# Optimization experiments

Measured on AMD Instinct MI355X. Metric: run time of the kernel, lower is better.

The kernel has to match this reference:

```python
import jax, jax.numpy as jnp
import numpy as np

DIM, HEADS, K_MAX, K_MIN = 512, 8, 32, 4
DH = DIM // HEADS


def _conv1x1(x, w, b=None):
    # 1x1 Conv2d == pointwise linear over channels: [B,C,H,W] x [O,C] -> [B,O,H,W]
    y = jnp.einsum('bchw,oc->bohw', x, w)
    if b is not None:
        y = y + b[None, :, None, None]
    return y


def setup_inputs() -> dict:
    key = jax.random.key(0)
    ks = jax.random.split(key, 8)
    B, C, H, W = 2, DIM, 64, 64
    s = lambda fan: 1.0 / np.sqrt(fan)
    x = jax.random.normal(ks[0], (B, C, H, W), jnp.float32)
    w_qkv = jax.random.normal(ks[1], (3 * C, C), jnp.float32) * s(C)   # qkv conv, bias=False
    w_proj = jax.random.normal(ks[2], (C, C), jnp.float32) * s(C)      # proj conv
    b_proj = jax.random.normal(ks[3], (C,), jnp.float32) * s(C)
    w_g1 = jax.random.normal(ks[4], (C // 4, C), jnp.float32) * s(C)   # gate conv 1
    b_g1 = jax.random.normal(ks[5], (C // 4,), jnp.float32) * s(C)
    w_g2 = jax.random.normal(ks[6], (1, C // 4), jnp.float32) * s(C // 4)  # gate conv 2
    b_g2 = jnp.full((1,), -1.0, jnp.float32)  # nn.init.constant_(gate[-2].bias, -1.0)
    return {"x": x, "w_qkv": w_qkv, "w_proj": w_proj, "b_proj": b_proj,
            "w_g1": w_g1, "b_g1": b_g1, "w_g2": w_g2, "b_g2": b_g2}


def reference(x, w_qkv, w_proj, b_proj, w_g1, b_g1, w_g2, b_g2):
    B, C, H, W = x.shape
    N = H * W
    qkv = _conv1x1(x, w_qkv)                              # [B,3C,H,W]
    q, k, v = jnp.split(qkv, 3, axis=1)

    def rs(t):  # [B,C,H,W] -> [B,heads,N,dh]
        return t.reshape(B, HEADS, DH, N).transpose(0, 1, 3, 2)

    q, k, v = rs(q), rs(k), rs(v)
    sim = jnp.einsum('bhid,bhjd->bhij', q, k) / np.sqrt(DH)  # [B,h,N,N]

    # adaptive tau gate -> per-query dynamic k
    tau = jax.nn.sigmoid(_conv1x1(jax.nn.relu(_conv1x1(x, w_g1, b_g1)), w_g2, b_g2))
    tau = tau.reshape(B, 1, N)
    k_dyn = jnp.clip((tau * K_MAX).astype(jnp.int32), K_MIN, K_MAX)  # [B,1,N]

    topk_val, topk_idx = jax.lax.top_k(sim, K_MAX)         # [B,h,N,K], sorted descending
    mask = jnp.arange(K_MAX)[None, None, None, :] < k_dyn[..., None]  # [B,1,N,K] (bcast over h)
    topk_val = jnp.where(mask, topk_val, -jnp.inf)
    attn = jax.nn.softmax(topk_val, axis=-1)               # [B,h,N,K]

    # gather values: gathered[b,h,i,kk,:] = v[b,h,topk_idx[b,h,i,kk],:]
    bi = jnp.arange(B)[:, None, None, None]
    hi = jnp.arange(HEADS)[None, :, None, None]
    gathered = v[bi, hi, topk_idx]                         # [B,h,N,K,dh]
    out = jnp.einsum('bhnk,bhnkd->bhnd', attn, gathered)   # [B,h,N,dh]

    out = out.transpose(0, 1, 3, 2).reshape(B, C, H, W)
    out = _conv1x1(out, w_proj, b_proj)                    # proj (proj_drop=0)
    return x + out
```

## Files before the change

### kernel.cpp

```cpp
#include <hip/hip_runtime.h>
#include <math.h>

#define XSTRIDE  2097152u
#define G1STRIDE 524288u

typedef _Float16 f16;
typedef f16   f16x8  __attribute__((ext_vector_type(8)));
typedef float f32x16 __attribute__((ext_vector_type(16)));
typedef unsigned int u32;
typedef unsigned short u16;

#define WS_QH 0u
#define WS_QL 2097152u
#define WS_KH 4194304u
#define WS_KL 6291456u
#define WS_VB 8388608u
#define WS_G1 10485760u
#define WS_KD 11534336u
#define WS_CI 11542528u

template<int EPI>
__global__ __launch_bounds__(256)
void gemm_kernel(const float* __restrict__ A, const float* __restrict__ B,
                 const float* __restrict__ bias, const float* __restrict__ resid,
                 void* P0, void* P1, void* P2, void* P3, void* P4)
{
    const int tid = threadIdx.x;
    const int tm = tid & 15;
    const int tn = tid >> 4;
    const int m0 = blockIdx.y * 128;
    const int n0 = blockIdx.x * 128;
    const int b  = blockIdx.z;

    const float* Bb = B + (size_t)b * XSTRIDE;

    __shared__ float As[16][132];
    __shared__ float Bs[16][132];

    float acc[8][8];
    #pragma unroll
    for (int i = 0; i < 8; ++i)
        #pragma unroll
        for (int j = 0; j < 8; ++j) acc[i][j] = 0.0f;

    for (int k0 = 0; k0 < 512; k0 += 16) {
        {
            int id = tid * 2;
            #pragma unroll
            for (int r = 0; r < 2; ++r, ++id) {
                int m = id >> 2, kq = (id & 3) * 4;
                float4 v = *(const float4*)(A + (size_t)(m0 + m) * 512 + k0 + kq);
                As[kq + 0][m] = v.x; As[kq + 1][m] = v.y;
                As[kq + 2][m] = v.z; As[kq + 3][m] = v.w;
            }
        }
        if (EPI != 2) {
            int id = tid * 2;
            #pragma unroll
            for (int r = 0; r < 2; ++r, ++id) {
                int kk = id >> 5, nq = (id & 31) * 4;
                *(float4*)(&Bs[kk][nq]) =
                    *(const float4*)(Bb + (size_t)(k0 + kk) * 4096 + n0 + nq);
            }
        } else {
            const float* O0p = (const float*)P1;
            const float* O1p = (const float*)P2;
            const int hh = k0 >> 6, d0 = k0 & 63;
            int id = tid * 2;
            #pragma unroll
            for (int r = 0; r < 2; ++r, ++id) {
                int n = id >> 2, kq = (id & 3) * 4;
                int dd = d0 + kq;
                size_t rowp = ((size_t)((b * 8 + hh) * 4096) + n0 + n) * 32;
                const float* src = (dd < 32) ? (O0p + rowp + dd) : (O1p + rowp + dd - 32);
                float4 v = *(const float4*)src;
                Bs[kq + 0][n] = v.x; Bs[kq + 1][n] = v.y;
                Bs[kq + 2][n] = v.z; Bs[kq + 3][n] = v.w;
            }
        }
        __syncthreads();
        #pragma unroll
        for (int k = 0; k < 16; ++k) {
            float4 a0 = *(const float4*)(&As[k][tm * 8]);
            float4 a1 = *(const float4*)(&As[k][tm * 8 + 4]);
            float4 b0 = *(const float4*)(&Bs[k][tn * 8]);
            float4 b1 = *(const float4*)(&Bs[k][tn * 8 + 4]);
            float a[8] = {a0.x, a0.y, a0.z, a0.w, a1.x, a1.y, a1.z, a1.w};
            float bb[8] = {b0.x, b0.y, b0.z, b0.w, b1.x, b1.y, b1.z, b1.w};
            #pragma unroll
            for (int i = 0; i < 8; ++i)
                #pragma unroll
                for (int j = 0; j < 8; ++j)
                    acc[i][j] += a[i] * bb[j];
        }
        __syncthreads();
    }

    if (EPI == 0) {
        const int which = m0 >> 9;
        const int mm = (m0 & 511) + tm * 8;
        const int hh = mm >> 6, d0 = mm & 63;
        const size_t rowbase = (size_t)((b * 8 + hh) * 4096);
        if (which == 2) {
            f16* VB = (f16*)P4;
            #pragma unroll
            for (int j = 0; j < 8; ++j) {
                int n = n0 + tn * 8 + j;
                f16x8 v;
                #pragma unroll
                for (int i = 0; i < 8; ++i) v[i] = (f16)acc[i][j];
                *(f16x8*)(VB + (rowbase + n) * 64 + d0) = v;
            }
        } else {
            f16* DH = (f16*)(which ? P2 : P0);
            f16* DL = (f16*)(which ? P3 : P1);
            const float scale = which ? 1.0f : 0.125f;
            #pragma unroll
            for (int j = 0; j < 8; ++j) {
                int n = n0 + tn * 8 + j;
                f16x8 vh, vl;
                #pragma unroll
                for (int i = 0; i < 8; ++i) {
                    float xx = acc[i][j] * scale;
                    f16 hs = (f16)xx;
                    vh[i] = hs;
                    vl[i] = (f16)((xx - (float)hs) * 4096.0f);
                }
                *(f16x8*)(DH + (rowbase + n) * 64 + d0) = vh;
                *(f16x8*)(DL + (rowbase + n) * 64 + d0) = vl;
            }
        }
    } else if (EPI == 1) {
        float* G1 = (float*)P0;
        #pragma unroll
        for (int i = 0; i < 8; ++i) {
            int o = tm * 8 + i;
            float bi = bias[o];
            float* dst = G1 + (size_t)b * G1STRIDE + (size_t)o * 4096 + n0 + tn * 8;
            float v[8];
            #pragma unroll
            for (int j = 0; j < 8; ++j) v[j] = fmaxf(acc[i][j] + bi, 0.0f);
            *(float4*)(dst) = make_float4(v[0], v[1], v[2], v[3]);
            *(float4*)(dst + 4) = make_float4(v[4], v[5], v[6], v[7]);
        }
    } else {
        float* out = (float*)P0;
        #pragma unroll
        for (int i = 0; i < 8; ++i) {
            int o = m0 + tm * 8 + i;
            float bi = bias[o];
            size_t off = (size_t)b * XSTRIDE + (size_t)o * 4096 + n0 + tn * 8;
            float4 r0 = *(const float4*)(resid + off);
            float4 r1 = *(const float4*)(resid + off + 4);
            *(float4*)(out + off) = make_float4(acc[i][0] + bi + r0.x, acc[i][1] + bi + r0.y,
                                                acc[i][2] + bi + r0.z, acc[i][3] + bi + r0.w);
            *(float4*)(out + off + 4) = make_float4(acc[i][4] + bi + r1.x, acc[i][5] + bi + r1.y,
                                                    acc[i][6] + bi + r1.z, acc[i][7] + bi + r1.w);
        }
    }
}

__global__ __launch_bounds__(256)
void convert_kernel(const float* __restrict__ x,
                    f16* __restrict__ XTH, f16* __restrict__ XTL)
{
    __shared__ float T[64][65];
    const int b = blockIdx.z;
    const int n0 = blockIdx.x * 64, k0 = blockIdx.y * 64;
    const int tid = threadIdx.x;
    const float* xb = x + (size_t)b * XSTRIDE;

    {
        const int c = tid & 63, r = tid >> 6;
        #pragma unroll
        for (int i = 0; i < 16; ++i)
            T[r + i * 4][c] = xb[(size_t)(k0 + r + i * 4) * 4096 + n0 + c];
    }
    __syncthreads();
    const int n = tid >> 2, a = tid & 3;
    f16x8 vh[2], vl[2];
    #pragma unroll
    for (int p = 0; p < 2; ++p)
        #pragma unroll
        for (int j = 0; j < 8; ++j) {
            float v = T[a * 16 + p * 8 + j][n];
            f16 h = (f16)v;
            vh[p][j] = h;
            vl[p][j] = (f16)((v - (float)h) * 4096.0f);
        }
    size_t dst = ((size_t)(b * 4096) + n0 + n) * 512 + k0 + a * 16;
    *(f16x8*)(XTH + dst)     = vh[0];
    *(f16x8*)(XTH + dst + 8) = vh[1];
    *(f16x8*)(XTL + dst)     = vl[0];
    *(f16x8*)(XTL + dst + 8) = vl[1];
}

__global__ __launch_bounds__(256, 2)
void qkv_gemm(const float* __restrict__ W, const f16* __restrict__ XTH,
              const f16* __restrict__ XTL,
              f16* __restrict__ QH, f16* __restrict__ QL,
              f16* __restrict__ KH, f16* __restrict__ KL,
              f16* __restrict__ VB)
{
    __shared__ __align__(16) char smem[33792];
    f16* Ah = (f16*)smem;
    f16* Al = (f16*)(smem + 6144);
    f16* Bh = (f16*)(smem + 12288);
    f16* Bl = (f16*)(smem + 18432);

    const int tid  = threadIdx.x;
    const int wid  = tid >> 6, lane = tid & 63;
    const int ln   = lane & 31, g = lane >> 5;
    const int wm   = wid >> 1, wn = wid & 1;
    const int m0   = blockIdx.y * 128;
    const int n0   = blockIdx.x * 128;
    const int b    = blockIdx.z;

    const int sm = tid >> 1, sko = (tid & 1) * 8;
    const float* wsrc  = W + (size_t)(m0 + sm) * 512 + sko;
    const f16*  bsrcH = XTH + ((size_t)(b * 4096) + n0 + sm) * 512 + sko;
    const f16*  bsrcL = XTL + ((size_t)(b * 4096) + n0 + sm) * 512 + sko;

    f32x16 accH[2][2], accL[2][2];
    #pragma unroll
    for (int rb = 0; rb < 2; ++rb)
        #pragma unroll
        for (int cb = 0; cb < 2; ++cb)
            #pragma unroll
            for (int r = 0; r < 16; ++r) { accH[rb][cb][r] = 0.0f; accL[rb][cb][r] = 0.0f; }

    for (int k0 = 0; k0 < 512; k0 += 16) {
        {
            float4 v0 = *(const float4*)(wsrc + k0);
            float4 v1 = *(const float4*)(wsrc + k0 + 4);
            float vv[8] = {v0.x, v0.y, v0.z, v0.w, v1.x, v1.y, v1.z, v1.w};
            f16x8 hh, ll;
            #pragma unroll
            for (int j = 0; j < 8; ++j) {
                f16 h = (f16)vv[j];
                hh[j] = h;
                ll[j] = (f16)((vv[j] - (float)h) * 4096.0f);
            }
            *(f16x8*)(Ah + sm * 24 + sko) = hh;
            *(f16x8*)(Al + sm * 24 + sko) = ll;
            *(f16x8*)(Bh + sm * 24 + sko) = *(const f16x8*)(bsrcH + k0);
            *(f16x8*)(Bl + sm * 24 + sko) = *(const f16x8*)(bsrcL + k0);
        }
        __syncthreads();
        f16x8 a_h[2], a_l[2], b_h[2], b_l[2];
        #pragma unroll
        for (int rb = 0; rb < 2; ++rb) {
            int row = wm * 64 + rb * 32 + ln;
            a_h[rb] = *(const f16x8*)(Ah + row * 24 + g * 8);
            a_l[rb] = *(const f16x8*)(Al + row * 24 + g * 8);
        }
        #pragma unroll
        for (int cb = 0; cb < 2; ++cb) {
            int col = wn * 64 + cb * 32 + ln;
            b_h[cb] = *(const f16x8*)(Bh + col * 24 + g * 8);
            b_l[cb] = *(const f16x8*)(Bl + col * 24 + g * 8);
        }
        #pragma unroll
        for (int rb = 0; rb < 2; ++rb)
            #pragma unroll
            for (int cb = 0; cb < 2; ++cb) {
                accH[rb][cb] = __builtin_amdgcn_mfma_f32_32x32x16_f16(a_h[rb], b_h[cb], accH[rb][cb], 0, 0, 0);
                accL[rb][cb] = __builtin_amdgcn_mfma_f32_32x32x16_f16(a_h[rb], b_l[cb], accL[rb][cb], 0, 0, 0);
                accL[rb][cb] = __builtin_amdgcn_mfma_f32_32x32x16_f16(a_l[rb], b_h[cb], accL[rb][cb], 0, 0, 0);
            }
        __syncthreads();
    }

    const int which = m0 >> 9;
    const float scale = (which == 0) ? 0.125f : 1.0f;
    const int hh_ = ((m0 & 511) >> 6) + wm;
    const size_t rowb0 = (size_t)(b * 8 + hh_) * 4096 + n0 + wn * 64 + lane;
    float* E = (float*)smem + wid * 2112;

    #pragma unroll
    for (int rb = 0; rb < 2; ++rb) {
        #pragma unroll
        for (int cb = 0; cb < 2; ++cb)
            #pragma unroll
            for (int r = 0; r < 16; ++r) {
                int row = (r & 3) + 8 * (r >> 2) + 4 * g;
                E[row * 66 + cb * 32 + ln] =
                    accH[rb][cb][r] + accL[rb][cb][r] * (1.0f / 4096.0f);
            }
        __syncthreads();
        const int dbase = rb * 32;
        if (which == 2) {
            #pragma unroll
            for (int oct = 0; oct < 4; ++oct) {
                f16x8 vv;
                #pragma unroll
                for (int j = 0; j < 8; ++j) vv[j] = (f16)E[(oct * 8 + j) * 66 + lane];
                *(f16x8*)(VB + rowb0 * 64 + dbase + oct * 8) = vv;
            }
        } else {
            f16* DH = which ? KH : QH;
            f16* DL = which ? KL : QL;
            #pragma unroll
            for (int oct = 0; oct < 4; ++oct) {
                f16x8 vh, vl;
                #pragma unroll
                for (int j = 0; j < 8; ++j) {
                    float xx = E[(oct * 8 + j) * 66 + lane] * scale;
                    f16 h = (f16)xx;
                    vh[j] = h;
                    vl[j] = (f16)((xx - (float)h) * 4096.0f);
                }
                *(f16x8*)(DH + rowb0 * 64 + dbase + oct * 8) = vh;
                *(f16x8*)(DL + rowb0 * 64 + dbase + oct * 8) = vl;
            }
        }
        __syncthreads();
    }
}

__global__ __launch_bounds__(64)
void gate2_kernel(const float* __restrict__ G1, const float* __restrict__ w2,
                  const float* __restrict__ b2, int* __restrict__ KD)
{
    const int b = blockIdx.y;
    const int n = blockIdx.x * 64 + threadIdx.x;
    const float* g = G1 + (size_t)b * G1STRIDE + n;
    float z = b2[0];
    #pragma unroll 8
    for (int c = 0; c < 128; ++c) z += w2[c] * g[(size_t)c * 4096];
    float tau = 1.0f / (1.0f + expf(-z));
    int kd = (int)(tau * 32.0f);
    kd = min(32, max(4, kd));
    KD[b * 4096 + n] = kd;
}

#define LOAD_BF(B0,B1,B2,B3,B4,B5,B6,B7, KHP, KLP, CB) do {                   \
    const f16* _ph = (KHP) + (size_t)((CB) * 32 + ln) * 64 + g * 8;           \
    const f16* _pl = (KLP) + (size_t)((CB) * 32 + ln) * 64 + g * 8;           \
    B0 = *(const f16x8*)(_ph);      B1 = *(const f16x8*)(_ph + 16);           \
    B2 = *(const f16x8*)(_ph + 32); B3 = *(const f16x8*)(_ph + 48);           \
    B4 = *(const f16x8*)(_pl);      B5 = *(const f16x8*)(_pl + 16);           \
    B6 = *(const f16x8*)(_pl + 32); B7 = *(const f16x8*)(_pl + 48);           \
} while (0)

#define P1_SCAN() do {                                                        \
    u32 _m = 0;                                                               \
    _Pragma("unroll")                                                         \
    for (int _q = 0; _q < 16; ++_q) {                                         \
        float2 _v = *(const float2*)(srow + 2 * _q);                          \
        _m |= (_v.x > thr) ? (1u << (2 * _q)) : 0u;                           \
        _m |= (_v.y > thr) ? (1u << (2 * _q + 1)) : 0u;                       \
    }                                                                         \
    while (__ballot(_m != 0u)) {                                              \
        bool _act = (_m != 0u);                                               \
        int _j = __builtin_ctz(_m ? _m : 1u);                                 \
        float _c = _act ? srow[_j] : 0.0f;                                    \
        _m &= (_m - 1u);                                                      \
        if (_act && _c > thr) {                                               \
            _Pragma("unroll")                                                 \
            for (int _r = 31; _r >= 1; --_r)                                  \
                L[_r] = __builtin_amdgcn_fmed3f(_c, L[_r - 1], L[_r]);        \
            L[0] = fmaxf(L[0], _c);                                           \
        }                                                                     \
    }                                                                         \
    {                                                                         \
        float _th = L[31];                                                    \
        _Pragma("unroll")                                                     \
        for (int _r = 30; _r >= 0; --_r) _th = (kdm1 == _r) ? L[_r] : _th;    \
        thr = _th;                                                            \
    }                                                                         \
} while (0)

#define P2_SCAN(JBASE) do {                                                   \
    u32 _m = 0;                                                               \
    _Pragma("unroll")                                                         \
    for (int _q = 0; _q < 16; ++_q) {                                         \
        float2 _v = *(const float2*)(srow + 2 * _q);                          \
        _m |= (_v.x >= theta) ? (1u << (2 * _q)) : 0u;                        \
        _m |= (_v.y >= theta) ? (1u << (2 * _q + 1)) : 0u;                    \
    }                                                                         \
    while (__ballot(_m != 0u)) {                                              \
        bool _act = (_m != 0u);                                               \
        int _j = __builtin_ctz(_m ? _m : 1u);                                 \
        float _c = _act ? srow[_j] : 0.0f;                                    \
        _m &= (_m - 1u);                                                      \
        if (_act) {                                                           \
            bool _isGT = _c > theta;                                          \
            bool _doA = (_isGT || eqc < eqNeed) && cnt < 32;                  \
            if (_doA) {                                                       \
                cvp[cnt] = _c;                                                \
                cip[cnt] = (u16)((JBASE) + _j);                               \
                cnt++;                                                        \
                if (!_isGT) eqc++;                                            \
            }                                                                 \
        }                                                                     \
    }                                                                         \
} while (0)

__device__ __forceinline__ void score_from(
    f16x8 bh0, f16x8 bh1, f16x8 bh2, f16x8 bh3,
    f16x8 bl0, f16x8 bl1, f16x8 bl2, f16x8 bl3,
    const f16x8 ah[2][4], const f16x8 al[2][4],
    float* __restrict__ Ss, int ln, int g)
{
    __builtin_amdgcn_s_setprio(1);
    #pragma unroll
    for (int rb = 0; rb < 2; ++rb) {
        f32x16 acc, accL;
        #pragma unroll
        for (int r = 0; r < 16; ++r) { acc[r] = 0.0f; accL[r] = 0.0f; }
        acc  = __builtin_amdgcn_mfma_f32_32x32x16_f16(ah[rb][0], bh0, acc,  0, 0, 0);
        accL = __builtin_amdgcn_mfma_f32_32x32x16_f16(al[rb][0], bh0, accL, 0, 0, 0);
        accL = __builtin_amdgcn_mfma_f32_32x32x16_f16(ah[rb][0], bl0, accL, 0, 0, 0);
        acc  = __builtin_amdgcn_mfma_f32_32x32x16_f16(ah[rb][1], bh1, acc,  0, 0, 0);
        accL = __builtin_amdgcn_mfma_f32_32x32x16_f16(al[rb][1], bh1, accL, 0, 0, 0);
        accL = __builtin_amdgcn_mfma_f32_32x32x16_f16(ah[rb][1], bl1, accL, 0, 0, 0);
        acc  = __builtin_amdgcn_mfma_f32_32x32x16_f16(ah[rb][2], bh2, acc,  0, 0, 0);
        accL = __builtin_amdgcn_mfma_f32_32x32x16_f16(al[rb][2], bh2, accL, 0, 0, 0);
        accL = __builtin_amdgcn_mfma_f32_32x32x16_f16(ah[rb][2], bl2, accL, 0, 0, 0);
        acc  = __builtin_amdgcn_mfma_f32_32x32x16_f16(ah[rb][3], bh3, acc,  0, 0, 0);
        accL = __builtin_amdgcn_mfma_f32_32x32x16_f16(al[rb][3], bh3, accL, 0, 0, 0);
        accL = __builtin_amdgcn_mfma_f32_32x32x16_f16(ah[rb][3], bl3, accL, 0, 0, 0);
        #pragma unroll
        for (int r = 0; r < 16; ++r) {
            int riw = rb * 32 + (r & 3) + 8 * (r >> 2) + 4 * g;
            Ss[riw * 34 + ln] = acc[r] + accL[r] * (1.0f / 4096.0f);
        }
    }
    __builtin_amdgcn_s_setprio(0);
}

__global__ __launch_bounds__(64)
__attribute__((amdgpu_waves_per_eu(2, 2)))
void select_kernel(const f16* __restrict__ QH, const f16* __restrict__ QL,
                   const f16* __restrict__ KH, const f16* __restrict__ KL,
                   const int* __restrict__ KD,
                   float* __restrict__ CV, u16* __restrict__ CI)
{
    const int qt = blockIdx.x >> 1;
    const int hf = blockIdx.x & 1;
    const int h = blockIdx.y, b = blockIdx.z;
    const size_t base = (size_t)((b * 8 + h) * 4096) * 64;
    const int lane = threadIdx.x;
    const int ln = lane & 31, g = lane >> 5;
    const int nw = qt * 64;
    const int k0base = hf * 2048;

    const int kd = KD[b * 4096 + nw + lane];
    const int kdm1 = kd - 1;

    __shared__ float Ss[64 * 34];

    f16x8 ah[2][4], al[2][4];
    #pragma unroll
    for (int rb = 0; rb < 2; ++rb) {
        const f16* ph = QH + base + (size_t)(nw + rb * 32 + ln) * 64 + g * 8;
        const f16* pl = QL + base + (size_t)(nw + rb * 32 + ln) * 64 + g * 8;
        #pragma unroll
        for (int s = 0; s < 4; ++s) {
            ah[rb][s] = *(const f16x8*)(ph + s * 16);
            al[rb][s] = *(const f16x8*)(pl + s * 16);
        }
    }

    const float INF = __builtin_inff();
    const float* srow = &Ss[lane * 34];

    f16x8 c0, c1, c2, c3, c4, c5, c6, c7;
    f16x8 n0, n1, n2, n3, n4, n5, n6, n7;

    float L[32];
    #pragma unroll
    for (int r = 0; r < 32; ++r) L[r] = -INF;
    float thr = -INF;

    {
        const f16* kh0 = KH + base + (size_t)k0base * 64;
        const f16* kl0 = KL + base + (size_t)k0base * 64;
        LOAD_BF(c0, c1, c2, c3, c4, c5, c6, c7, kh0, kl0, 0);
        for (int t = 0; t < 32; ++t) {
            const f16* kh_t = KH + base + (size_t)(k0base + t * 64) * 64;
            const f16* kl_t = KL + base + (size_t)(k0base + t * 64) * 64;
            const int t1 = (t < 31) ? t + 1 : 31;
            const f16* kh_n = KH + base + (size_t)(k0base + t1 * 64) * 64;
            const f16* kl_n = KL + base + (size_t)(k0base + t1 * 64) * 64;
            LOAD_BF(n0, n1, n2, n3, n4, n5, n6, n7, kh_t, kl_t, 1);
            score_from(c0, c1, c2, c3, c4, c5, c6, c7, ah, al, Ss, ln, g);
            P1_SCAN();
            LOAD_BF(c0, c1, c2, c3, c4, c5, c6, c7, kh_n, kl_n, 0);
            score_from(n0, n1, n2, n3, n4, n5, n6, n7, ah, al, Ss, ln, g);
            P1_SCAN();
        }
    }
    const float theta = thr;
    int cntGT = 0;
    #pragma unroll
    for (int r = 0; r < 32; ++r) cntGT += ((r < kd) && (L[r] > theta)) ? 1 : 0;
    const int eqNeed = kd - cntGT;

    const size_t crow = (size_t)((b * 8 + h) * 4096 + nw + lane);
    float* cvp = CV + crow * 64 + hf * 32;
    u16*   cip = CI + crow * 64 + hf * 32;
    int cnt = 0, eqc = 0;

    {
        const f16* kh0 = KH + base + (size_t)k0base * 64;
        const f16* kl0 = KL + base + (size_t)k0base * 64;
        LOAD_BF(c0, c1, c2, c3, c4, c5, c6, c7, kh0, kl0, 0);
        for (int t = 0; t < 32; ++t) {
            const f16* kh_t = KH + base + (size_t)(k0base + t * 64) * 64;
            const f16* kl_t = KL + base + (size_t)(k0base + t * 64) * 64;
            const int t1 = (t < 31) ? t + 1 : 31;
            const f16* kh_n = KH + base + (size_t)(k0base + t1 * 64) * 64;
            const f16* kl_n = KL + base + (size_t)(k0base + t1 * 64) * 64;
            LOAD_BF(n0, n1, n2, n3, n4, n5, n6, n7, kh_t, kl_t, 1);
            score_from(c0, c1, c2, c3, c4, c5, c6, c7, ah, al, Ss, ln, g);
            P2_SCAN(k0base + t * 64);
            LOAD_BF(c0, c1, c2, c3, c4, c5, c6, c7, kh_n, kl_n, 0);
            score_from(n0, n1, n2, n3, n4, n5, n6, n7, ah, al, Ss, ln, g);
            P2_SCAN(k0base + t * 64 + 32);
        }
    }
}

__global__ __launch_bounds__(64)
void merge_kernel(const float* __restrict__ CV, const u16* __restrict__ CI,
                  const int* __restrict__ KD, const f16* __restrict__ VB,
                  float* __restrict__ O0, float* __restrict__ O1)
{
    const int tid = threadIdx.x;
    const size_t R0 = (size_t)blockIdx.x * 64;

    __shared__ float Lv[64][66];
    __shared__ u16   Li[64][66];
    __shared__ float Mv[64][34];
    __shared__ u16   Mi[64][34];

    for (int i = 0; i < 64; ++i) {
        Lv[i][tid] = CV[(R0 + i) * 64 + tid];
        Li[i][tid] = CI[(R0 + i) * 64 + tid];
    }
    __syncthreads();

    const int myR = (int)R0 + tid;
    const int b = myR >> 15, n = myR & 4095, h = (myR >> 12) & 7;
    const int kd = KD[b * 4096 + n];

    const float INF = __builtin_inff();
    float L[32]; int I[32];
    #pragma unroll
    for (int r = 0; r < 32; ++r) { L[r] = -INF; I[r] = 0; }

    for (int i = 0; i < 64; ++i) {
        float c = Lv[tid][i];
        int  ix = Li[tid][i];
        if (c > L[31]) {
            #pragma unroll
            for (int r = 31; r >= 1; --r) {
                bool gp = c > L[r - 1];
                bool gc = c > L[r];
                L[r] = gp ? L[r - 1] : (gc ? c : L[r]);
                I[r] = gp ? I[r - 1] : (gc ? ix : I[r]);
            }
            if (c > L[0]) { I[0] = ix; L[0] = c; }
        }
    }

    #pragma unroll
    for (int r = 0; r < 32; ++r) { Mv[tid][r] = L[r]; Mi[tid][r] = (u16)I[r]; }

    const float mx = Mv[tid][0];
    float sum = 0.0f;
    for (int k = 0; k < kd; ++k) {
        float e = expf(Mv[tid][k] - mx);
        Mv[tid][k] = e;
        sum += e;
    }
    const float inv = 1.0f / sum;

    float o[64];
    #pragma unroll
    for (int d = 0; d < 64; ++d) o[d] = 0.0f;
    const size_t vbase = (size_t)((b * 8 + h)) * 4096 * 64;
    for (int k = 0; k < kd; ++k) {
        float wgt = Mv[tid][k] * inv;
        const f16* vp = VB + vbase + (size_t)Mi[tid][k] * 64;
        #pragma unroll
        for (int part = 0; part < 8; ++part) {
            f16x8 vv = *(const f16x8*)(vp + part * 8);
            #pragma unroll
            for (int e2 = 0; e2 < 8; ++e2) o[part * 8 + e2] += wgt * (float)vv[e2];
        }
    }

    __syncthreads();
    #pragma unroll
    for (int q = 0; q < 32; ++q)
        *(float2*)(&Lv[tid][2 * q]) = make_float2(o[2 * q], o[2 * q + 1]);
    __syncthreads();
    for (int i = 0; i < 64; ++i) {
        float val = Lv[i][tid];
        size_t R = R0 + i;
        if (tid < 32) O0[R * 32 + tid] = val;
        else          O1[R * 32 + (tid - 32)] = val;
    }
}

extern "C" void kernel_launch(void* const* d_in, const int* in_sizes, int n_in,
                              void* d_out, int out_size, void* d_ws, size_t ws_size,
                              hipStream_t stream)
{
    const float* x      = (const float*)d_in[0];
    const float* w_qkv  = (const float*)d_in[1];
    const float* w_proj = (const float*)d_in[2];
    const float* b_proj = (const float*)d_in[3];
    const float* w_g1   = (const float*)d_in[4];
    const float* b_g1   = (const float*)d_in[5];
    const float* w_g2   = (const float*)d_in[6];
    const float* b_g2   = (const float*)d_in[7];
    float* out = (float*)d_out;
    float* ws  = (float*)d_ws;

    f16* QH = (f16*)(ws + WS_QH);
    f16* QL = (f16*)(ws + WS_QL);
    f16* KH = (f16*)(ws + WS_KH);
    f16* KL = (f16*)(ws + WS_KL);
    f16* VB = (f16*)(ws + WS_VB);
    float* G1 = ws + WS_G1;
    int*   KD = (int*)(ws + WS_KD);
    u16*   CI = (u16*)(ws + WS_CI);
    float* CV = out;
    float* O0 = (float*)QH;
    float* O1 = (float*)QL;

    f16* XTH = (f16*)out;
    f16* XTL = (f16*)out + 4194304;

    convert_kernel<<<dim3(64, 8, 2), 256, 0, stream>>>(x, XTH, XTL);
    qkv_gemm<<<dim3(32, 12, 2), 256, 0, stream>>>(
        w_qkv, XTH, XTL, QH, QL, KH, KL, VB);
    gemm_kernel<1><<<dim3(32, 1, 2), 256, 0, stream>>>(
        w_g1, x, b_g1, nullptr, G1, nullptr, nullptr, nullptr, nullptr);

    hipMemsetAsync(CV, 0xFF, (size_t)out_size * sizeof(float), stream);

    gate2_kernel<<<dim3(64, 2), 64, 0, stream>>>(G1, w_g2, b_g2, KD);
    select_kernel<<<dim3(128, 8, 2), 64, 0, stream>>>(QH, QL, KH, KL, KD, CV, CI);
    merge_kernel<<<dim3(1024), 64, 0, stream>>>(CV, CI, KD, VB, O0, O1);
    gemm_kernel<2><<<dim3(32, 4, 2), 256, 0, stream>>>(
        w_proj, nullptr, b_proj, x, out, O0, O1, nullptr, nullptr);
}
```

Baseline: 665.0 us.

## Split each query row's key scan across two half-waves in select kernel

The select kernel now handles 32 queries per wave instead of 64. Each query row's 32 scores per block are split between the two 32-lane halves, so each lane scans only 16 candidates. After the first pass the two per-half top-32 lists are merged with a cross-lane shuffle and a bitonic-style max/min network to derive the threshold. In the second pass the halves write candidates from opposite ends of the 32-slot buffer. The grid doubles, the explicit double-buffered K prefetch is removed, and the waves-per-EU hint is raised to target more occupancy. The aim is more parallelism and shorter serial scan loops, at the cost of twice the Q-fragment loads, no software prefetch, and the risk that the two halves' slot writes collide if their combined count exceeds 32.

```diff
diff --git a/kernel.cpp b/kernel.cpp
--- a/kernel.cpp
+++ b/kernel.cpp
@@ -334,19 +334,10 @@
     KD[b * 4096 + n] = kd;
 }
 
-#define LOAD_BF(B0,B1,B2,B3,B4,B5,B6,B7, KHP, KLP, CB) do {                   \
-    const f16* _ph = (KHP) + (size_t)((CB) * 32 + ln) * 64 + g * 8;           \
-    const f16* _pl = (KLP) + (size_t)((CB) * 32 + ln) * 64 + g * 8;           \
-    B0 = *(const f16x8*)(_ph);      B1 = *(const f16x8*)(_ph + 16);           \
-    B2 = *(const f16x8*)(_ph + 32); B3 = *(const f16x8*)(_ph + 48);           \
-    B4 = *(const f16x8*)(_pl);      B5 = *(const f16x8*)(_pl + 16);           \
-    B6 = *(const f16x8*)(_pl + 32); B7 = *(const f16x8*)(_pl + 48);           \
-} while (0)
-
 #define P1_SCAN() do {                                                        \
     u32 _m = 0;                                                               \
     _Pragma("unroll")                                                         \
-    for (int _q = 0; _q < 16; ++_q) {                                         \
+    for (int _q = 0; _q < 8; ++_q) {                                          \
         float2 _v = *(const float2*)(srow + 2 * _q);                          \
         _m |= (_v.x > thr) ? (1u << (2 * _q)) : 0u;                           \
         _m |= (_v.y > thr) ? (1u << (2 * _q + 1)) : 0u;                       \
@@ -374,7 +365,7 @@
 #define P2_SCAN(JBASE) do {                                                   \
     u32 _m = 0;                                                               \
     _Pragma("unroll")                                                         \
-    for (int _q = 0; _q < 16; ++_q) {                                         \
+    for (int _q = 0; _q < 8; ++_q) {                                          \
         float2 _v = *(const float2*)(srow + 2 * _q);                          \
         _m |= (_v.x >= theta) ? (1u << (2 * _q)) : 0u;                        \
         _m |= (_v.y >= theta) ? (1u << (2 * _q + 1)) : 0u;                    \
@@ -388,8 +379,9 @@
             bool _isGT = _c > theta;                                          \
             bool _doA = (_isGT || eqc < eqNeed) && cnt < 32;                  \
             if (_doA) {                                                       \
-                cvp[cnt] = _c;                                                \
-                cip[cnt] = (u16)((JBASE) + _j);                               \
+                int _sl = g ? (31 - cnt) : cnt;                               \
+                cvp[_sl] = _c;                                                \
+                cip[_sl] = (u16)((JBASE) + _j);                               \
                 cnt++;                                                        \
                 if (!_isGT) eqc++;                                            \
             }                                                                 \
@@ -397,41 +389,33 @@
     }                                                                         \
 } while (0)
 
-__device__ __forceinline__ void score_from(
-    f16x8 bh0, f16x8 bh1, f16x8 bh2, f16x8 bh3,
-    f16x8 bl0, f16x8 bl1, f16x8 bl2, f16x8 bl3,
-    const f16x8 ah[2][4], const f16x8 al[2][4],
+__device__ __forceinline__ void score32(
+    const f16* __restrict__ kh_t, const f16* __restrict__ kl_t, int cb,
+    const f16x8 ah[4], const f16x8 al[4],
     float* __restrict__ Ss, int ln, int g)
 {
     __builtin_amdgcn_s_setprio(1);
-    #pragma unroll
-    for (int rb = 0; rb < 2; ++rb) {
-        f32x16 acc, accL;
-        #pragma unroll
-        for (int r = 0; r < 16; ++r) { acc[r] = 0.0f; accL[r] = 0.0f; }
-        acc  = __builtin_amdgcn_mfma_f32_32x32x16_f16(ah[rb][0], bh0, acc,  0, 0, 0);
-        accL = __builtin_amdgcn_mfma_f32_32x32x16_f16(al[rb][0], bh0, accL, 0, 0, 0);
-        accL = __builtin_amdgcn_mfma_f32_32x32x16_f16(ah[rb][0], bl0, accL, 0, 0, 0);
-        acc  = __builtin_amdgcn_mfma_f32_32x32x16_f16(ah[rb][1], bh1, acc,  0, 0, 0);
-        accL = __builtin_amdgcn_mfma_f32_32x32x16_f16(al[rb][1], bh1, accL, 0, 0, 0);
-        accL = __builtin_amdgcn_mfma_f32_32x32x16_f16(ah[rb][1], bl1, accL, 0, 0, 0);
-        acc  = __builtin_amdgcn_mfma_f32_32x32x16_f16(ah[rb][2], bh2, acc,  0, 0, 0);
-        accL = __builtin_amdgcn_mfma_f32_32x32x16_f16(al[rb][2], bh2, accL, 0, 0, 0);
-        accL = __builtin_amdgcn_mfma_f32_32x32x16_f16(ah[rb][2], bl2, accL, 0, 0, 0);
-        acc  = __builtin_amdgcn_mfma_f32_32x32x16_f16(ah[rb][3], bh3, acc,  0, 0, 0);
-        accL = __builtin_amdgcn_mfma_f32_32x32x16_f16(al[rb][3], bh3, accL, 0, 0, 0);
-        accL = __builtin_amdgcn_mfma_f32_32x32x16_f16(ah[rb][3], bl3, accL, 0, 0, 0);
-        #pragma unroll
-        for (int r = 0; r < 16; ++r) {
-            int riw = rb * 32 + (r & 3) + 8 * (r >> 2) + 4 * g;
-            Ss[riw * 34 + ln] = acc[r] + accL[r] * (1.0f / 4096.0f);
-        }
+    f32x16 acc, accL;
+    #pragma unroll
+    for (int r = 0; r < 16; ++r) { acc[r] = 0.0f; accL[r] = 0.0f; }
+    #pragma unroll
+    for (int s = 0; s < 4; ++s) {
+        f16x8 bh = *(const f16x8*)(kh_t + (size_t)(cb * 32 + ln) * 64 + s * 16 + g * 8);
+        f16x8 bl = *(const f16x8*)(kl_t + (size_t)(cb * 32 + ln) * 64 + s * 16 + g * 8);
+        acc  = __builtin_amdgcn_mfma_f32_32x32x16_f16(ah[s], bh, acc,  0, 0, 0);
+        accL = __builtin_amdgcn_mfma_f32_32x32x16_f16(al[s], bh, accL, 0, 0, 0);
+        accL = __builtin_amdgcn_mfma_f32_32x32x16_f16(ah[s], bl, accL, 0, 0, 0);
+    }
+    #pragma unroll
+    for (int r = 0; r < 16; ++r) {
+        int riw = (r & 3) + 8 * (r >> 2) + 4 * g;
+        Ss[riw * 34 + ln] = acc[r] + accL[r] * (1.0f / 4096.0f);
     }
     __builtin_amdgcn_s_setprio(0);
 }
 
 __global__ __launch_bounds__(64)
-__attribute__((amdgpu_waves_per_eu(2, 2)))
+__attribute__((amdgpu_waves_per_eu(3, 4)))
 void select_kernel(const f16* __restrict__ QH, const f16* __restrict__ QL,
                    const f16* __restrict__ KH, const f16* __restrict__ KL,
                    const int* __restrict__ KD,
@@ -443,83 +427,84 @@
     const size_t base = (size_t)((b * 8 + h) * 4096) * 64;
     const int lane = threadIdx.x;
     const int ln = lane & 31, g = lane >> 5;
-    const int nw = qt * 64;
+    const int nw = qt * 32;
     const int k0base = hf * 2048;
 
-    const int kd = KD[b * 4096 + nw + lane];
+    const int kd = KD[b * 4096 + nw + ln];
     const int kdm1 = kd - 1;
 
-    __shared__ float Ss[64 * 34];
-
-    f16x8 ah[2][4], al[2][4];
-    #pragma unroll
-    for (int rb = 0; rb < 2; ++rb) {
-        const f16* ph = QH + base + (size_t)(nw + rb * 32 + ln) * 64 + g * 8;
-        const f16* pl = QL + base + (size_t)(nw + rb * 32 + ln) * 64 + g * 8;
+    __shared__ float Ss[32 * 34];
+
+    f16x8 ah[4], al[4];
+    {
+        const f16* ph = QH + base + (size_t)(nw + ln) * 64 + g * 8;
+        const f16* pl = QL + base + (size_t)(nw + ln) * 64 + g * 8;
         #pragma unroll
         for (int s = 0; s < 4; ++s) {
-            ah[rb][s] = *(const f16x8*)(ph + s * 16);
-            al[rb][s] = *(const f16x8*)(pl + s * 16);
+            ah[s] = *(const f16x8*)(ph + s * 16);
+            al[s] = *(const f16x8*)(pl + s * 16);
         }
     }
 
     const float INF = __builtin_inff();
-    const float* srow = &Ss[lane * 34];
-
-    f16x8 c0, c1, c2, c3, c4, c5, c6, c7;
-    f16x8 n0, n1, n2, n3, n4, n5, n6, n7;
+    const float* srow = &Ss[ln * 34 + g * 16];
 
     float L[32];
     #pragma unroll
     for (int r = 0; r < 32; ++r) L[r] = -INF;
     float thr = -INF;
 
+    for (int t = 0; t < 32; ++t) {
+        const f16* kh_t = KH + base + (size_t)(k0base + t * 64) * 64;
+        const f16* kl_t = KL + base + (size_t)(k0base + t * 64) * 64;
+        score32(kh_t, kl_t, 0, ah, al, Ss, ln, g);
+        P1_SCAN();
+        score32(kh_t, kl_t, 1, ah, al, Ss, ln, g);
+        P1_SCAN();
+    }
+
+    float M[32];
+    #pragma unroll
+    for (int i = 0; i < 32; ++i) {
+        float p = __shfl_xor(L[31 - i], 32, 64);
+        M[i] = fmaxf(L[i], p);
+    }
+    #pragma unroll
+    for (int d = 16; d >= 1; d >>= 1) {
+        #pragma unroll
+        for (int i = 0; i < 32; ++i) {
+            if (!(i & d) && (i + d) < 32) {
+                float a = M[i], b2 = M[i + d];
+                M[i] = fmaxf(a, b2);
+                M[i + d] = fminf(a, b2);
+            }
+        }
+    }
+
+    float theta;
     {
-        const f16* kh0 = KH + base + (size_t)k0base * 64;
-        const f16* kl0 = KL + base + (size_t)k0base * 64;
-        LOAD_BF(c0, c1, c2, c3, c4, c5, c6, c7, kh0, kl0, 0);
-        for (int t = 0; t < 32; ++t) {
-            const f16* kh_t = KH + base + (size_t)(k0base + t * 64) * 64;
-            const f16* kl_t = KL + base + (size_t)(k0base + t * 64) * 64;
-            const int t1 = (t < 31) ? t + 1 : 31;
-            const f16* kh_n = KH + base + (size_t)(k0base + t1 * 64) * 64;
-            const f16* kl_n = KL + base + (size_t)(k0base + t1 * 64) * 64;
-            LOAD_BF(n0, n1, n2, n3, n4, n5, n6, n7, kh_t, kl_t, 1);
-            score_from(c0, c1, c2, c3, c4, c5, c6, c7, ah, al, Ss, ln, g);
-            P1_SCAN();
-            LOAD_BF(c0, c1, c2, c3, c4, c5, c6, c7, kh_n, kl_n, 0);
-            score_from(n0, n1, n2, n3, n4, n5, n6, n7, ah, al, Ss, ln, g);
-            P1_SCAN();
-        }
-    }
-    const float theta = thr;
+        float th = M[31];
+        #pragma unroll
+        for (int r = 30; r >= 0; --r) th = (kdm1 == r) ? M[r] : th;
+        theta = th;
+    }
     int cntGT = 0;
     #pragma unroll
-    for (int r = 0; r < 32; ++r) cntGT += ((r < kd) && (L[r] > theta)) ? 1 : 0;
+    for (int r = 0; r < 32; ++r) cntGT += ((r < kd) && (M[r] > theta)) ? 1 : 0;
     const int eqNeed = kd - cntGT;
 
-    const size_t crow = (size_t)((b * 8 + h) * 4096 + nw + lane);
+    const size_t crow = (size_t)((b * 8 + h) * 4096 + nw + ln);
     float* cvp = CV + crow * 64 + hf * 32;
     u16*   cip = CI + crow * 64 + hf * 32;
     int cnt = 0, eqc = 0;
 
-    {
-        const f16* kh0 = KH + base + (size_t)k0base * 64;
-        const f16* kl0 = KL + base + (size_t)k0base * 64;
-        LOAD_BF(c0, c1, c2, c3, c4, c5, c6, c7, kh0, kl0, 0);
-        for (int t = 0; t < 32; ++t) {
-            const f16* kh_t = KH + base + (size_t)(k0base + t * 64) * 64;
-            const f16* kl_t = KL + base + (size_t)(k0base + t * 64) * 64;
-            const int t1 = (t < 31) ? t + 1 : 31;
-            const f16* kh_n = KH + base + (size_t)(k0base + t1 * 64) * 64;
-            const f16* kl_n = KL + base + (size_t)(k0base + t1 * 64) * 64;
-            LOAD_BF(n0, n1, n2, n3, n4, n5, n6, n7, kh_t, kl_t, 1);
-            score_from(c0, c1, c2, c3, c4, c5, c6, c7, ah, al, Ss, ln, g);
-            P2_SCAN(k0base + t * 64);
-            LOAD_BF(c0, c1, c2, c3, c4, c5, c6, c7, kh_n, kl_n, 0);
-            score_from(n0, n1, n2, n3, n4, n5, n6, n7, ah, al, Ss, ln, g);
-            P2_SCAN(k0base + t * 64 + 32);
-        }
+    for (int t = 0; t < 32; ++t) {
+        const f16* kh_t = KH + base + (size_t)(k0base + t * 64) * 64;
+        const f16* kl_t = KL + base + (size_t)(k0base + t * 64) * 64;
+        score32(kh_t, kl_t, 0, ah, al, Ss, ln, g);
+        P2_SCAN(k0base + t * 64 + g * 16);
+        score32(kh_t, kl_t, 1, ah, al, Ss, ln, g);
+        P2_SCAN(k0base + t * 64 + 32 + g * 16);
     }
 }
 
@@ -645,7 +630,7 @@
     hipMemsetAsync(CV, 0xFF, (size_t)out_size * sizeof(float), stream);
 
     gate2_kernel<<<dim3(64, 2), 64, 0, stream>>>(G1, w_g2, b_g2, KD);
-    select_kernel<<<dim3(128, 8, 2), 64, 0, stream>>>(QH, QL, KH, KL, KD, CV, CI);
+    select_kernel<<<dim3(256, 8, 2), 64, 0, stream>>>(QH, QL, KH, KL, KD, CV, CI);
     merge_kernel<<<dim3(1024), 64, 0, stream>>>(CV, CI, KD, VB, O0, O1);
     gemm_kernel<2><<<dim3(32, 4, 2), 256, 0, stream>>>(
         w_proj, nullptr, b_proj, x, out, O0, O1, nullptr, nullptr);
```

Result: slower. 928.9 us (+39.7%).
